# Kernel optimization log

Hardware: AMD Instinct MI355X
Metric: run time of the kernel (lower is better)

Reference implementation:

```python
import jax, jax.numpy as jnp
import numpy as np


def _lin(x, w, b=None):
    # torch nn.Linear convention: y = x @ W^T + b, W: (out, in)
    y = jnp.einsum('...d,ed->...e', x, w)
    return y + b if b is not None else y


def setup_inputs() -> dict:
    key = jax.random.key(0)
    B, N, M, d = 8, 256, 128, 128
    ks = jax.random.split(key, 20)
    sc = 1.0 / np.sqrt(d)
    inp = {
        's': jax.random.normal(ks[0], (B, N, d), jnp.float32),
        'v': jax.random.normal(ks[1], (B, N, M, d), jnp.float32),
        'gs': jax.random.normal(ks[2], (B, d), jnp.float32),
        'gv': jax.random.normal(ks[3], (B, M, d), jnp.float32),
        'gv2': jax.random.normal(ks[4], (B, M, M, d), jnp.float32),
        'lin1_w': jax.random.normal(ks[5], (d, d), jnp.float32) * sc,
        'lin1_b': jax.random.normal(ks[6], (d,), jnp.float32) * sc,
        'lin2_w': jax.random.normal(ks[7], (d, d), jnp.float32) * sc,
        'lin2_b': jax.random.normal(ks[8], (d,), jnp.float32) * sc,
        'lin3_w': jax.random.normal(ks[9], (d, d), jnp.float32) * sc,
        'lin3_b': jax.random.normal(ks[10], (d,), jnp.float32) * sc,
        'linv1_w': jax.random.normal(ks[11], (d, d), jnp.float32) * sc,
        'linv2_w': jax.random.normal(ks[12], (d, d), jnp.float32) * sc,
        'linv3_w': jax.random.normal(ks[13], (d, d), jnp.float32) * sc,
        'mlp_w1': jax.random.normal(ks[14], (d, d), jnp.float32) * sc,
        'mlp_b1': jax.random.normal(ks[15], (d,), jnp.float32) * sc,
        'mlp_w2': jax.random.normal(ks[16], (d, d), jnp.float32) * sc,
        'mlp_b2': jax.random.normal(ks[17], (d,), jnp.float32) * sc,
    }
    return inp


def reference(s, v, gs, gv, gv2,
              lin1_w, lin1_b, lin2_w, lin2_b, lin3_w, lin3_b,
              linv1_w, linv2_w, linv3_w,
              mlp_w1, mlp_b1, mlp_w2, mlp_b2):
    # v update: three (B,N,M,d) branches, averaged
    v_vv2 = _lin(jnp.einsum('bnmd,bmcd->bncd', v, gv2), linv1_w)
    v_vs = _lin(gs[:, None, None, :] * v, linv3_w)
    v_sv = _lin(s[:, :, None, :] * gv[:, None, :, :], linv2_w)
    v_new = (v_vv2 + v_sv + v_vs) / 3
    # s update
    s_v2t = jnp.einsum('bmmd->bd', gv2)                 # per-channel trace of gv2
    s_vv = jnp.einsum('bmd,bnmd->bnd', gv, v_new)
    s_new = ((_lin(s_v2t, lin1_w, lin1_b) * gs)[:, None, :]
             * _lin(s, lin2_w, lin2_b)
             * _lin(s_vv, lin3_w, lin3_b))
    # MLP: Linear -> ReLU -> Linear
    s_new = _lin(jax.nn.relu(_lin(s_new, mlp_w1, mlp_b1)), mlp_w2, mlp_b2)
    return (s_new, v_new)
```

## Files before the change

kernel.cpp:

```cpp
#include <hip/hip_runtime.h>
#include <hip/hip_bf16.h>
#include <stdint.h>

#define B_ 8
#define N_ 256
#define M_ 128
#define D_ 128

typedef __attribute__((ext_vector_type(8))) short short8;
typedef __attribute__((ext_vector_type(4))) short short4v;
typedef __attribute__((ext_vector_type(4))) float f32x4;

static __device__ __forceinline__ unsigned short f2bf(float x) {
    union { float f; unsigned int u; } c; c.f = x;
    unsigned int r = (c.u + 0x7FFFu + ((c.u >> 16) & 1u)) >> 16;
    return (unsigned short)r;
}
static __device__ __forceinline__ unsigned short bfhu(float x) {
    union { float f; unsigned int u; } c; c.f = x;
    return (unsigned short)((c.u + 0x8000u) >> 16);
}
static __device__ __forceinline__ unsigned int pkhu(float a, float b) {
    union { float f; unsigned int u; } ca, cb; ca.f = a; cb.f = b;
    return ((ca.u + 0x8000u) >> 16) | ((cb.u + 0x8000u) & 0xFFFF0000u);
}

__global__ void k0a_prep(const float* __restrict__ lin2_w, const float* __restrict__ lin3_w,
                         const float* __restrict__ mlp_w1, const float* __restrict__ mlp_w2,
                         const float* __restrict__ linv1_w, const float* __restrict__ linv2_w,
                         const float* __restrict__ linv3_w,
                         float* __restrict__ wT2, float* __restrict__ wT3,
                         float* __restrict__ wTm1, float* __restrict__ wTm2,
                         unsigned short* __restrict__ wfrag) {
    int gid = blockIdx.x * 256 + threadIdx.x;
    int task = gid >> 14;
    int idx = gid & 16383;
    if (task < 4) {
        int e = idx & 127, dd = idx >> 7;
        const float* src = task == 0 ? lin2_w : task == 1 ? lin3_w : task == 2 ? mlp_w1 : mlp_w2;
        float* dst = task == 0 ? wT2 : task == 1 ? wT3 : task == 2 ? wTm1 : wTm2;
        dst[dd * 128 + e] = src[e * 128 + dd];
    } else {
        int mat = task - 4;
        const float* src = mat == 0 ? linv1_w : mat == 1 ? linv2_w : linv3_w;
        int e = idx >> 7, k = idx & 127;
        int dst = ((((e >> 4) * 12 + (mat * 4 + (k >> 5))) * 4 + ((k >> 3) & 3)) * 16 + (e & 15)) * 8
                  + (k & 7);
        wfrag[dst] = f2bf(src[idx] * (1.0f / 3.0f));
    }
}

__global__ void k0b_trace(const float* __restrict__ gv2, float* __restrict__ s_v2t) {
    int b = blockIdx.x, d = threadIdx.x;
    const float* p = gv2 + (size_t)b * (M_ * M_ * D_) + d;
    float acc = 0.f;
    #pragma unroll 8
    for (int m = 0; m < 128; ++m) acc += p[(size_t)m * 16512];
    s_v2t[b * 128 + d] = acc;
}

__global__ void k0c_g1(const float* __restrict__ s_v2t, const float* __restrict__ lin1_w,
                       const float* __restrict__ lin1_b, const float* __restrict__ gs,
                       float* __restrict__ g1) {
    __shared__ float sv[128];
    int b = blockIdx.x, e = threadIdx.x;
    sv[e] = s_v2t[b * 128 + e];
    __syncthreads();
    const float* w = lin1_w + e * 128;
    float acc = 0.f;
    #pragma unroll 4
    for (int dd = 0; dd < 128; ++dd) acc = fmaf(sv[dd], w[dd], acc);
    g1[b * 128 + e] = (acc + lin1_b[e]) * gs[b * 128 + e];
}

__global__ __launch_bounds__(256) void kt_v(const float* __restrict__ v,
                                            unsigned short* __restrict__ vT) {
    __shared__ unsigned short tl[128 * 136];
    int bid = blockIdx.x;
    int b = bid >> 8;
    int R0 = (bid & 255) * 128;
    int t = threadIdx.x;
    const float* src = v + ((size_t)b * 32768 + R0) * 128;
    #pragma unroll
    for (int i = 0; i < 16; ++i) {
        int flat = i * 256 + t;
        int row = flat >> 5, slot = flat & 31;
        float4 x = *(const float4*)(src + (size_t)row * 128 + slot * 4);
        #pragma unroll
        for (int j = 0; j < 4; ++j) {
            int d = slot * 4 + j;
            tl[d * 136 + (row ^ (((d >> 2) & 7) << 3))] = bfhu(((const float*)&x)[j]);
        }
    }
    __syncthreads();
    #pragma unroll
    for (int i = 0; i < 8; ++i) {
        int flat = i * 256 + t;
        int d = flat >> 4, rs = flat & 15;
        short8 y = *(const short8*)&tl[d * 136 + ((rs * 8) ^ (((d >> 2) & 7) << 3))];
        *(short8*)(vT + (size_t)(b * 128 + d) * 32768 + R0 + rs * 8) = y;
    }
}

__global__ __launch_bounds__(256) void kt_g(const float* __restrict__ gv2,
                                            unsigned short* __restrict__ gT) {
    __shared__ unsigned short tl[128 * 136];
    int bid = blockIdx.x;
    int b = bid >> 7;
    int c = bid & 127;
    int t = threadIdx.x;
    const float* src = gv2 + ((size_t)(b * 128) * 128 + c) * 128;
    #pragma unroll
    for (int i = 0; i < 16; ++i) {
        int flat = i * 256 + t;
        int m = flat >> 5, slot = flat & 31;
        float4 x = *(const float4*)(src + (size_t)m * 16384 + slot * 4);
        #pragma unroll
        for (int j = 0; j < 4; ++j) {
            int d = slot * 4 + j;
            tl[d * 136 + (m ^ (((d >> 2) & 7) << 3))] = bfhu(((const float*)&x)[j]);
        }
    }
    __syncthreads();
    #pragma unroll
    for (int i = 0; i < 8; ++i) {
        int flat = i * 256 + t;
        int d = flat >> 4, ms = flat & 15;
        short8 y = *(const short8*)&tl[d * 136 + ((ms * 8) ^ (((d >> 2) & 7) << 3))];
        *(short8*)(gT + ((size_t)(b * 128 + d) * 128 + c) * 128 + ms * 8) = y;
    }
}

__global__ __launch_bounds__(512, 2) void k1_T2_fast(const unsigned short* __restrict__ vT,
                                                     const unsigned short* __restrict__ gT,
                                                     unsigned short* __restrict__ t2base) {
    __shared__ unsigned short sm[40960];
    int bid = blockIdx.x;
    int b = bid & 7;
    int r = bid >> 3;
    int nt = r & 3, ch = (r >> 2) & 1, dc = r >> 3;
    int n0 = nt * 64, c0 = ch * 64, d0 = dc * 8;
    int t = threadIdx.x;
    int w = t >> 6, lane = t & 63, ln15 = lane & 15, kg = lane >> 4;

    f32x4 acc[4][4];
    #pragma unroll
    for (int i = 0; i < 4; ++i)
        #pragma unroll
        for (int j = 0; j < 4; ++j) acc[i][j] = (f32x4){0.f, 0.f, 0.f, 0.f};

    for (int mc = 0; mc < 4; ++mc) {
        int m0 = mc * 32;
        #pragma unroll
        for (int i = 0; i < 4; ++i) {
            int flat = i * 512 + t;
            int d = flat >> 8, x = (flat >> 2) & 63, ms = flat & 3;
            short8 a = *(const short8*)(vT + ((size_t)(b * 128 + d0 + d) * 256 + n0 + x) * 128
                                           + m0 + ms * 8);
            *(short8*)&sm[d * 2560 + x * 40 + ms * 8] = a;
            short8 g = *(const short8*)(gT + ((size_t)(b * 128 + d0 + d) * 128 + c0 + x) * 128
                                           + m0 + ms * 8);
            *(short8*)&sm[20480 + d * 2560 + x * 40 + ms * 8] = g;
        }
        __syncthreads();
        short8 af[4], bf[4];
        #pragma unroll
        for (int i = 0; i < 4; ++i)
            af[i] = *(const short8*)&sm[w * 2560 + (i * 16 + ln15) * 40 + kg * 8];
        #pragma unroll
        for (int j = 0; j < 4; ++j)
            bf[j] = *(const short8*)&sm[20480 + w * 2560 + (j * 16 + ln15) * 40 + kg * 8];
        #pragma unroll
        for (int i = 0; i < 4; ++i)
            #pragma unroll
            for (int j = 0; j < 4; ++j)
                acc[i][j] = __builtin_amdgcn_mfma_f32_16x16x32_bf16(af[i], bf[j], acc[i][j], 0, 0, 0);
        __syncthreads();
    }
    #pragma unroll
    for (int i = 0; i < 4; ++i)
        #pragma unroll
        for (int j = 0; j < 4; ++j)
            #pragma unroll
            for (int q = 0; q < 4; ++q) {
                int n = i * 16 + kg * 4 + q;
                int c = j * 16 + ln15;
                sm[n * 520 + c * 8 + w] = bfhu(acc[i][j][q]);
            }
    __syncthreads();
    #pragma unroll
    for (int p = 0; p < 8; ++p) {
        int u = p * 512 + t;
        int n = u >> 6;
        int c = u & 63;
        short8 x = *(const short8*)&sm[n * 520 + c * 8];
        size_t kb = (size_t)(b * N_ + n0 + n) * 2 + ch;
        *(short8*)(t2base + kb * 16384 + (size_t)((c >> 4) * 16 + dc) * 128 + (c & 15) * 8) = x;
    }
}

__global__ __launch_bounds__(512, 4) void k1_T2_legacy(const float* __restrict__ v,
                                                       const float* __restrict__ gv2,
                                                       unsigned short* __restrict__ t2base) {
    __shared__ unsigned short sm[40960];
    int bid = blockIdx.x;
    int b = bid & 7;
    int r = bid >> 3;
    int nt = r & 3, ch = (r >> 2) & 1, dc = r >> 3;
    int n0 = nt * 64, c0 = ch * 64, d0 = dc * 8;
    int t = threadIdx.x;
    int w = t >> 6, lane = t & 63, ln15 = lane & 15, kg = lane >> 4;

    f32x4 acc[4][4];
    #pragma unroll
    for (int i = 0; i < 4; ++i)
        #pragma unroll
        for (int j = 0; j < 4; ++j) acc[i][j] = (f32x4){0.f, 0.f, 0.f, 0.f};

    int d0l = (t & 1) * 4;
    int am = (t >> 1) & 31, anb = t >> 6;
    int bc = (t >> 1) & 63, bmb = t >> 7;

    for (int mc = 0; mc < 4; ++mc) {
        int m0 = mc * 32;
        {
            const float* src = v + (((size_t)(b * N_ + n0) * M_ + m0 + am) * D_ + d0 + d0l);
            #pragma unroll
            for (int p = 0; p < 8; ++p) {
                int n = p * 8 + anb;
                float4 x = *(const float4*)(src + (size_t)n * (M_ * D_));
                #pragma unroll
                for (int j = 0; j < 4; ++j)
                    sm[(d0l + j) * 2560 + n * 40 + am] = f2bf(((const float*)&x)[j]);
            }
        }
        {
            const float* src = gv2 + (((size_t)(b * M_ + m0) * M_ + c0 + bc) * D_ + d0 + d0l);
            #pragma unroll
            for (int p = 0; p < 8; ++p) {
                int m = p * 4 + bmb;
                float4 x = *(const float4*)(src + (size_t)m * (M_ * D_));
                #pragma unroll
                for (int j = 0; j < 4; ++j)
                    sm[20480 + (d0l + j) * 2560 + bc * 40 + m] = f2bf(((const float*)&x)[j]);
            }
        }
        __syncthreads();
        short8 af[4], bf[4];
        #pragma unroll
        for (int i = 0; i < 4; ++i)
            af[i] = *(const short8*)&sm[w * 2560 + (i * 16 + ln15) * 40 + kg * 8];
        #pragma unroll
        for (int j = 0; j < 4; ++j)
            bf[j] = *(const short8*)&sm[20480 + w * 2560 + (j * 16 + ln15) * 40 + kg * 8];
        #pragma unroll
        for (int i = 0; i < 4; ++i)
            #pragma unroll
            for (int j = 0; j < 4; ++j)
                acc[i][j] = __builtin_amdgcn_mfma_f32_16x16x32_bf16(af[i], bf[j], acc[i][j], 0, 0, 0);
        __syncthreads();
    }
    #pragma unroll
    for (int i = 0; i < 4; ++i)
        #pragma unroll
        for (int j = 0; j < 4; ++j)
            #pragma unroll
            for (int q = 0; q < 4; ++q) {
                int n = i * 16 + kg * 4 + q;
                int c = j * 16 + ln15;
                sm[(n * 64 + c) * 8 + w] = f2bf(acc[i][j][q]);
            }
    __syncthreads();
    #pragma unroll
    for (int p = 0; p < 8; ++p) {
        int u = p * 512 + t;
        int n = u >> 6;
        int c = u & 63;
        short8 x = *(const short8*)&sm[(n * 64 + c) * 8];
        size_t kb = (size_t)(b * N_ + n0 + n) * 2 + ch;
        *(short8*)(t2base + kb * 16384 + (size_t)((c >> 4) * 16 + dc) * 128 + (c & 15) * 8) = x;
    }
}

__global__ __launch_bounds__(512, 4) void k2_vnew_w(
        const float* __restrict__ s, const float* __restrict__ v,
        const float* __restrict__ gs, const float* __restrict__ gv,
        const unsigned short* __restrict__ wfrag,
        float* __restrict__ vnew, float* __restrict__ svv) {
    __shared__ unsigned short lds_a[6144];
    int t = threadIdx.x;
    int kb2 = blockIdx.x;
    int b = kb2 >> 8;
    int w = t >> 6, lane = t & 63, ln15 = lane & 15, kgrp = lane >> 4;
    int ct = w;

    f32x4 wreg[12];
    #pragma unroll
    for (int kk = 0; kk < 12; ++kk)
        wreg[kk] = *(const f32x4*)&wfrag[(((ct * 12 + kk) * 4 + kgrp) * 16 + ln15) * 8];
    asm volatile("" : "+v"(wreg[0]), "+v"(wreg[1]), "+v"(wreg[2]), "+v"(wreg[3]),
                      "+v"(wreg[4]), "+v"(wreg[5]), "+v"(wreg[6]), "+v"(wreg[7]),
                      "+v"(wreg[8]), "+v"(wreg[9]), "+v"(wreg[10]), "+v"(wreg[11]));

    int r_s = t >> 5;
    int q5 = t & 31;
    int dd0 = q5 * 4;
    float4 s4  = *(const float4*)(s + (size_t)kb2 * 128 + dd0);
    float4 gs4 = *(const float4*)(gs + (size_t)b * 128 + dd0);
    const float* gvb = gv + (size_t)b * 16384;
    const unsigned short* t2u = (const unsigned short*)(vnew + (size_t)kb2 * 16384);
    float* outp = vnew + (size_t)kb2 * 16384;
    int lw = 2048 + (q5 >> 3) * 512 + ((q5 >> 1) & 3) * 128 + r_s * 8 + (q5 & 1) * 4;

    float psum = 0.f;
    #pragma unroll
    for (int j = 0; j < 8; ++j) {
        int rt = (0x45760132u >> (4 * j)) & 7;
        int crow = (rt >> 2) * 64 + (rt & 3) * 16;
        if (t < 256) {
            short8 x = *(const short8*)(t2u + (rt >> 2) * 16384 + (rt & 3) * 2048 + t * 8);
            *(short8*)&lds_a[t * 8] = x;
        }
        {
            float4 g4 = *(const float4*)(gvb + (size_t)(crow + r_s) * 128 + dd0);
            uint2 p = make_uint2(pkhu(s4.x * g4.x, s4.y * g4.y),
                                 pkhu(s4.z * g4.z, s4.w * g4.w));
            *(uint2*)&lds_a[lw] = p;
        }
        {
            float4 v4 = *(const float4*)(v + ((size_t)kb2 * 128 + crow + r_s) * 128 + dd0);
            uint2 p = make_uint2(pkhu(gs4.x * v4.x, gs4.y * v4.y),
                                 pkhu(gs4.z * v4.z, gs4.w * v4.w));
            *(uint2*)&lds_a[lw + 2048] = p;
        }
        __syncthreads();
        f32x4 acc = {0.f, 0.f, 0.f, 0.f};
        #pragma unroll
        for (int kk = 0; kk < 12; ++kk) {
            short8 a = *(const short8*)&lds_a[kk * 512 + kgrp * 128 + ln15 * 8];
            acc = __builtin_amdgcn_mfma_f32_16x16x32_bf16(
                a, __builtin_bit_cast(short8, wreg[kk]), acc, 0, 0, 0);
        }
        int e = ct * 16 + ln15;
        #pragma unroll
        for (int q = 0; q < 4; ++q) {
            int row = crow + kgrp * 4 + q;
            outp[(size_t)row * 128 + e] = acc[q];
            psum = fmaf(gvb[(size_t)row * 128 + e], acc[q], psum);
        }
        __syncthreads();
    }
    psum += __shfl_xor(psum, 16);
    psum += __shfl_xor(psum, 32);
    if (kgrp == 0) svv[(size_t)kb2 * 128 + ct * 16 + ln15] = psum;
}

__global__ __launch_bounds__(256) void k4_spath(
        const float* __restrict__ s, const float* __restrict__ svv,
        const float* __restrict__ g1,
        const float* __restrict__ wT2, const float* __restrict__ lin2_b,
        const float* __restrict__ wT3, const float* __restrict__ lin3_b,
        const float* __restrict__ wTm1, const float* __restrict__ mlp_b1,
        const float* __restrict__ wTm2, const float* __restrict__ mlp_b2,
        float* __restrict__ sout) {
    __shared__ float xs[8][128], xv[8][128], pre[8][128], hbuf[8][128];
    int t = threadIdx.x;
    int rowb = blockIdx.x * 8;
    int b = rowb >> 8;
    #pragma unroll
    for (int i = 0; i < 4; ++i) {
        int vi = i * 256 + t;
        int r = vi >> 7, dd = vi & 127;
        xs[r][dd] = s[(size_t)(rowb + r) * 128 + dd];
        xv[r][dd] = svv[(size_t)(rowb + r) * 128 + dd];
    }
    __syncthreads();
    int e = t & 127, h2 = t >> 7;
    float b2 = lin2_b[e], b3 = lin3_b[e], g1v = g1[b * 128 + e];
    float a2[4] = {b2, b2, b2, b2}, a3[4] = {b3, b3, b3, b3};
    for (int dd = 0; dd < 128; ++dd) {
        float w2 = wT2[dd * 128 + e], w3 = wT3[dd * 128 + e];
        #pragma unroll
        for (int r = 0; r < 4; ++r) {
            a2[r] = fmaf(xs[h2 * 4 + r][dd], w2, a2[r]);
            a3[r] = fmaf(xv[h2 * 4 + r][dd], w3, a3[r]);
        }
    }
    #pragma unroll
    for (int r = 0; r < 4; ++r) pre[h2 * 4 + r][e] = g1v * a2[r] * a3[r];
    __syncthreads();
    float bm1 = mlp_b1[e];
    float ah[4] = {bm1, bm1, bm1, bm1};
    for (int dd = 0; dd < 128; ++dd) {
        float w = wTm1[dd * 128 + e];
        #pragma unroll
        for (int r = 0; r < 4; ++r) ah[r] = fmaf(pre[h2 * 4 + r][dd], w, ah[r]);
    }
    #pragma unroll
    for (int r = 0; r < 4; ++r) hbuf[h2 * 4 + r][e] = fmaxf(ah[r], 0.f);
    __syncthreads();
    float bm2 = mlp_b2[e];
    float ao[4] = {bm2, bm2, bm2, bm2};
    for (int dd = 0; dd < 128; ++dd) {
        float w = wTm2[dd * 128 + e];
        #pragma unroll
        for (int r = 0; r < 4; ++r) ao[r] = fmaf(hbuf[h2 * 4 + r][dd], w, ao[r]);
    }
    #pragma unroll
    for (int r = 0; r < 4; ++r) sout[(size_t)(rowb + h2 * 4 + r) * 128 + e] = ao[r];
}

extern "C" void kernel_launch(void* const* d_in, const int* in_sizes, int n_in,
                              void* d_out, int out_size, void* d_ws, size_t ws_size,
                              hipStream_t stream) {
    const float* s       = (const float*)d_in[0];
    const float* v       = (const float*)d_in[1];
    const float* gs      = (const float*)d_in[2];
    const float* gv      = (const float*)d_in[3];
    const float* gv2     = (const float*)d_in[4];
    const float* lin1_w  = (const float*)d_in[5];
    const float* lin1_b  = (const float*)d_in[6];
    const float* lin2_w  = (const float*)d_in[7];
    const float* lin2_b  = (const float*)d_in[8];
    const float* lin3_w  = (const float*)d_in[9];
    const float* lin3_b  = (const float*)d_in[10];
    const float* linv1_w = (const float*)d_in[11];
    const float* linv2_w = (const float*)d_in[12];
    const float* linv3_w = (const float*)d_in[13];
    const float* mlp_w1  = (const float*)d_in[14];
    const float* mlp_b1  = (const float*)d_in[15];
    const float* mlp_w2  = (const float*)d_in[16];
    const float* mlp_b2  = (const float*)d_in[17];

    float* sout = (float*)d_out;
    float* vnew = (float*)d_out + 262144;

    float* wsf   = (float*)d_ws;
    float* wT2   = wsf;
    float* wT3   = wsf + 16384;
    float* wTm1  = wsf + 32768;
    float* wTm2  = wsf + 49152;
    float* s_v2t = wsf + 65536;
    float* g1    = wsf + 66560;
    float* svv   = wsf + 67584;
    unsigned short* wfrag = (unsigned short*)(wsf + 329728);
    unsigned short* vT  = (unsigned short*)((char*)d_ws + 2097152);
    unsigned short* gT  = (unsigned short*)((char*)d_ws + 69206016);
    bool big = ws_size >= 102760448ULL;

    k0a_prep<<<448, 256, 0, stream>>>(lin2_w, lin3_w, mlp_w1, mlp_w2,
                                      linv1_w, linv2_w, linv3_w,
                                      wT2, wT3, wTm1, wTm2, wfrag);
    k0b_trace<<<8, 128, 0, stream>>>(gv2, s_v2t);
    k0c_g1<<<8, 128, 0, stream>>>(s_v2t, lin1_w, lin1_b, gs, g1);
    if (big) {
        kt_v<<<2048, 256, 0, stream>>>(v, vT);
        kt_g<<<1024, 256, 0, stream>>>(gv2, gT);
        k1_T2_fast<<<1024, 512, 0, stream>>>(vT, gT, (unsigned short*)vnew);
    } else {
        k1_T2_legacy<<<1024, 512, 0, stream>>>(v, gv2, (unsigned short*)vnew);
    }
    k2_vnew_w<<<2048, 512, 0, stream>>>(s, v, gs, gv, wfrag, vnew, svv);
    k4_spath<<<256, 256, 0, stream>>>(s, svv, g1, wT2, lin2_b, wT3, lin3_b,
                                      wTm1, mlp_b1, wTm2, mlp_b2, sout);
}
```

Before: 258.9 us.

## Double-buffer LDS in k2_vnew_w with register prefetch and XOR swizzle

The k2 loop now issues the global loads for the next row tile into registers before running the MFMA chain on the current tile, and writes them into a second LDS buffer afterwards. This hides global-load latency behind compute. It also XOR-swizzles the LDS row offsets to cut bank conflicts on the short8 reads and writes. LDS use doubles to about 24KB per block, which may limit occupancy at 4 blocks per CU, and the loop still has two barriers per iteration.

After: 252.8 us. 1.02x faster.

```diff
diff --git a/kernel.cpp b/kernel.cpp
--- a/kernel.cpp
+++ b/kernel.cpp
@@ -287,7 +287,7 @@
         const float* __restrict__ gs, const float* __restrict__ gv,
         const unsigned short* __restrict__ wfrag,
         float* __restrict__ vnew, float* __restrict__ svv) {
-    __shared__ unsigned short lds_a[6144];
+    __shared__ unsigned short lds_a[2][6144];
     int t = threadIdx.x;
     int kb2 = blockIdx.x;
     int b = kb2 >> 8;
@@ -305,42 +305,53 @@
     int r_s = t >> 5;
     int q5 = t & 31;
     int dd0 = q5 * 4;
+    int kgq = (q5 >> 1) & 3;
+    int lw = (q5 >> 3) * 512 + kgq * 128 + ((r_s ^ kgq) * 8) + (q5 & 1) * 4;
+    int st2 = (t * 8) ^ (((t >> 4) & 3) << 3);
+
     float4 s4  = *(const float4*)(s + (size_t)kb2 * 128 + dd0);
     float4 gs4 = *(const float4*)(gs + (size_t)b * 128 + dd0);
     const float* gvb = gv + (size_t)b * 16384;
     const unsigned short* t2u = (const unsigned short*)(vnew + (size_t)kb2 * 16384);
     float* outp = vnew + (size_t)kb2 * 16384;
-    int lw = 2048 + (q5 >> 3) * 512 + ((q5 >> 1) & 3) * 128 + r_s * 8 + (q5 & 1) * 4;
-
+
+    short8 t2r;
+    float4 g4, v4;
     float psum = 0.f;
+
+    {
+        int rt = 2;
+        int crow = (rt >> 2) * 64 + (rt & 3) * 16;
+        if (t < 256) t2r = *(const short8*)(t2u + (rt >> 2) * 16384 + (rt & 3) * 2048 + t * 8);
+        g4 = *(const float4*)(gvb + (size_t)(crow + r_s) * 128 + dd0);
+        v4 = *(const float4*)(v + ((size_t)kb2 * 128 + crow + r_s) * 128 + dd0);
+        if (t < 256) *(short8*)&lds_a[0][st2] = t2r;
+        uint2 p1 = make_uint2(pkhu(s4.x * g4.x, s4.y * g4.y), pkhu(s4.z * g4.z, s4.w * g4.w));
+        *(uint2*)&lds_a[0][2048 + lw] = p1;
+        uint2 p2 = make_uint2(pkhu(gs4.x * v4.x, gs4.y * v4.y), pkhu(gs4.z * v4.z, gs4.w * v4.w));
+        *(uint2*)&lds_a[0][4096 + lw] = p2;
+    }
+    __syncthreads();
+
     #pragma unroll
     for (int j = 0; j < 8; ++j) {
         int rt = (0x45760132u >> (4 * j)) & 7;
-        int crow = (rt >> 2) * 64 + (rt & 3) * 16;
-        if (t < 256) {
-            short8 x = *(const short8*)(t2u + (rt >> 2) * 16384 + (rt & 3) * 2048 + t * 8);
-            *(short8*)&lds_a[t * 8] = x;
-        }
-        {
-            float4 g4 = *(const float4*)(gvb + (size_t)(crow + r_s) * 128 + dd0);
-            uint2 p = make_uint2(pkhu(s4.x * g4.x, s4.y * g4.y),
-                                 pkhu(s4.z * g4.z, s4.w * g4.w));
-            *(uint2*)&lds_a[lw] = p;
-        }
-        {
-            float4 v4 = *(const float4*)(v + ((size_t)kb2 * 128 + crow + r_s) * 128 + dd0);
-            uint2 p = make_uint2(pkhu(gs4.x * v4.x, gs4.y * v4.y),
-                                 pkhu(gs4.z * v4.z, gs4.w * v4.w));
-            *(uint2*)&lds_a[lw + 2048] = p;
-        }
-        __syncthreads();
+        int cur = j & 1;
+        if (j < 7) {
+            int rtn = (0x45760132u >> (4 * (j + 1))) & 7;
+            int crn = (rtn >> 2) * 64 + (rtn & 3) * 16;
+            if (t < 256) t2r = *(const short8*)(t2u + (rtn >> 2) * 16384 + (rtn & 3) * 2048 + t * 8);
+            g4 = *(const float4*)(gvb + (size_t)(crn + r_s) * 128 + dd0);
+            v4 = *(const float4*)(v + ((size_t)kb2 * 128 + crn + r_s) * 128 + dd0);
+        }
         f32x4 acc = {0.f, 0.f, 0.f, 0.f};
         #pragma unroll
         for (int kk = 0; kk < 12; ++kk) {
-            short8 a = *(const short8*)&lds_a[kk * 512 + kgrp * 128 + ln15 * 8];
+            short8 a = *(const short8*)&lds_a[cur][kk * 512 + kgrp * 128 + ((ln15 ^ kgrp) * 8)];
             acc = __builtin_amdgcn_mfma_f32_16x16x32_bf16(
                 a, __builtin_bit_cast(short8, wreg[kk]), acc, 0, 0, 0);
         }
+        int crow = (rt >> 2) * 64 + (rt & 3) * 16;
         int e = ct * 16 + ln15;
         #pragma unroll
         for (int q = 0; q < 4; ++q) {
@@ -348,7 +359,16 @@
             outp[(size_t)row * 128 + e] = acc[q];
             psum = fmaf(gvb[(size_t)row * 128 + e], acc[q], psum);
         }
-        __syncthreads();
+        if (j < 7) {
+            __syncthreads();
+            if (t < 256) *(short8*)&lds_a[cur ^ 1][st2] = t2r;
+            uint2 p1 = make_uint2(pkhu(s4.x * g4.x, s4.y * g4.y), pkhu(s4.z * g4.z, s4.w * g4.w));
+            *(uint2*)&lds_a[cur ^ 1][2048 + lw] = p1;
+            uint2 p2 = make_uint2(pkhu(gs4.x * v4.x, gs4.y * v4.y),
+                                  pkhu(gs4.z * v4.z, gs4.w * v4.w));
+            *(uint2*)&lds_a[cur ^ 1][4096 + lw] = p2;
+            __syncthreads();
+        }
     }
     psum += __shfl_xor(psum, 16);
     psum += __shfl_xor(psum, 32);
```
